# Performance work log

Measured on AMD Instinct MI355X. Metric: run time of the kernel, lower is better.

Reference implementation:

```python
import jax, jax.numpy as jnp
import numpy as np

NUM_HEADS = 6
KERNEL = 5
EPS = 1e-6


def _neighbor_idx(L, k):
    # NATTEN neighborhood: window start clamped so every query has exactly k neighbors
    starts = jnp.clip(jnp.arange(L) - k // 2, 0, L - k)
    return starts[:, None] + jnp.arange(k)  # [L, k]


def ada_rmsnorm(x, scale, w1, b1, w2, b2):
    # x: [B,C,D,H,W]; RMS over spatial dims, gamma from channel means via small MLP
    rms = jnp.sqrt(jnp.mean(x * x, axis=(2, 3, 4), keepdims=True) + EPS)
    xn = x / rms
    stats = jnp.mean(x, axis=(2, 3, 4))                 # [B,C]
    h = jax.nn.relu(stats @ w1.T + b1)                  # [B,2C]
    gamma = jax.nn.sigmoid(h @ w2.T + b2)               # [B,C]
    return xn * (scale * gamma[:, :, None, None, None])


def reference(x, scale1, n1_w1, n1_b1, n1_w2, n1_b2,
              qkv_w, qkv_b, proj_w, proj_b,
              scale2, n2_w1, n2_b1, n2_w2, n2_b2,
              mlp_w1, mlp_b1, mlp_w2, mlp_b2):
    B, C, D, H, W = x.shape
    nh_, k_ = NUM_HEADS, KERNEL
    hd = C // nh_
    K3 = k_ ** 3

    # --- norm1 + neighborhood attention ---
    h = ada_rmsnorm(x, scale1, n1_w1, n1_b1, n1_w2, n1_b2)
    t = jnp.transpose(h, (0, 2, 3, 4, 1))               # [B,D,H,W,C]
    qkv = t @ qkv_w.T + qkv_b                           # [B,D,H,W,3C]
    q, k, v = jnp.split(qkv, 3, axis=-1)
    q = q.reshape(B, D, H, W, nh_, hd)
    k = k.reshape(B, D, H, W, nh_, hd)
    v = v.reshape(B, D, H, W, nh_, hd)

    iD = _neighbor_idx(D, k_)
    iH = _neighbor_idx(H, k_)
    iW = _neighbor_idx(W, k_)
    nd = iD[:, None, None, :, None, None]               # [D,1,1,k,1,1]
    nhh = iH[None, :, None, None, :, None]              # [1,H,1,1,k,1]
    nw = iW[None, None, :, None, None, :]               # [1,1,W,1,1,k]

    k_nb = k[:, nd, nhh, nw].reshape(B, D, H, W, K3, nh_, hd)
    v_nb = v[:, nd, nhh, nw].reshape(B, D, H, W, K3, nh_, hd)

    scale_qk = hd ** -0.5
    scores = jnp.einsum('bdhwnc,bdhwknc->bdhwnk', q, k_nb) * scale_qk  # [B,D,H,W,heads,K3]
    p = jax.nn.softmax(scores, axis=-1)
    o = jnp.einsum('bdhwnk,bdhwknc->bdhwnc', p, v_nb).reshape(B, D, H, W, C)
    o = o @ proj_w.T + proj_b                            # output projection
    x = x + jnp.transpose(o, (0, 4, 1, 2, 3))

    # --- norm2 + 1x1-conv MLP (GELU exact) ---
    h2 = ada_rmsnorm(x, scale2, n2_w1, n2_b1, n2_w2, n2_b2)
    m = jnp.einsum('oc,bcdhw->bodhw', mlp_w1, h2) + mlp_b1[None, :, None, None, None]
    m = jax.nn.gelu(m, approximate=False)
    m = jnp.einsum('oc,bcdhw->bodhw', mlp_w2, m) + mlp_b2[None, :, None, None, None]
    return x + m


def setup_inputs() -> dict:
    key = jax.random.key(0)
    ks = jax.random.split(key, 16)
    B, C, D, H, W = 1, 192, 16, 16, 16
    hid = 2 * C
    mlp_h = int(4.0 * C)
    s = 0.02
    inp = {
        'x': jax.random.normal(ks[0], (B, C, D, H, W), jnp.float32),
        'scale1': jnp.ones((1, C, 1, 1, 1), jnp.float32),
        'n1_w1': jax.random.normal(ks[1], (hid, C), jnp.float32) * s,
        'n1_b1': jnp.zeros((hid,), jnp.float32),
        'n1_w2': jax.random.normal(ks[2], (C, hid), jnp.float32) * s,
        'n1_b2': jnp.zeros((C,), jnp.float32),
        'qkv_w': jax.random.normal(ks[3], (3 * C, C), jnp.float32) * s,
        'qkv_b': jnp.zeros((3 * C,), jnp.float32),
        'proj_w': jax.random.normal(ks[4], (C, C), jnp.float32) * s,
        'proj_b': jnp.zeros((C,), jnp.float32),
        'scale2': jnp.ones((1, C, 1, 1, 1), jnp.float32),
        'n2_w1': jax.random.normal(ks[5], (hid, C), jnp.float32) * s,
        'n2_b1': jnp.zeros((hid,), jnp.float32),
        'n2_w2': jax.random.normal(ks[6], (C, hid), jnp.float32) * s,
        'n2_b2': jnp.zeros((C,), jnp.float32),
        'mlp_w1': jax.random.normal(ks[7], (mlp_h, C), jnp.float32) * s,
        'mlp_b1': jnp.zeros((mlp_h,), jnp.float32),
        'mlp_w2': jax.random.normal(ks[8], (C, mlp_h), jnp.float32) * s,
        'mlp_b2': jnp.zeros((C,), jnp.float32),
    }
    return inp
```

## Files before the change

kernel.cpp:

```cpp
#include <hip/hip_runtime.h>
#include <hip/hip_bf16.h>
#include <cmath>


#define NPOS 4096
#define C_CH 192

typedef __bf16 bf16x8 __attribute__((ext_vector_type(8)));
typedef __bf16 bf16x4 __attribute__((ext_vector_type(4)));
typedef float  f32x4  __attribute__((ext_vector_type(4)));

__global__ __launch_bounds__(256) void stats_kernel(
    const float* __restrict__ x, float* __restrict__ sums, float* __restrict__ sumsq)
{
    int c = blockIdx.x;
    const float4* xc = (const float4*)(x + (size_t)c * NPOS);
    float s = 0.f, s2 = 0.f;
    for (int i = threadIdx.x; i < NPOS / 4; i += 256) {
        float4 v = xc[i];
        s  += v.x + v.y + v.z + v.w;
        s2 += v.x * v.x + v.y * v.y + v.z * v.z + v.w * v.w;
    }
    #pragma unroll
    for (int off = 32; off > 0; off >>= 1) {
        s  += __shfl_down(s, off);
        s2 += __shfl_down(s2, off);
    }
    __shared__ float ls[4], ls2[4];
    int wid = threadIdx.x >> 6;
    if ((threadIdx.x & 63) == 0) { ls[wid] = s; ls2[wid] = s2; }
    __syncthreads();
    if (threadIdx.x == 0) {
        float t = 0.f, t2 = 0.f;
        #pragma unroll
        for (int w = 0; w < 4; w++) { t += ls[w]; t2 += ls2[w]; }
        sums[c] = t; sumsq[c] = t2;
    }
}

__global__ __launch_bounds__(384) void gamma_kernel(
    const float* __restrict__ sums, const float* __restrict__ sumsq,
    const float* __restrict__ scale,
    const float* __restrict__ w1, const float* __restrict__ b1,
    const float* __restrict__ w2, const float* __restrict__ b2,
    float* __restrict__ gs)
{
    __shared__ float stats[C_CH];
    __shared__ float h[384];
    int t = threadIdx.x;
    if (t < C_CH) stats[t] = sums[t] * (1.0f / (float)NPOS);
    __syncthreads();
    {
        float acc = b1[t];
        const float* wr = w1 + (size_t)t * C_CH;
        #pragma unroll 4
        for (int c = 0; c < C_CH; c += 4) {
            float4 w4 = *(const float4*)(wr + c);
            acc += w4.x * stats[c] + w4.y * stats[c + 1] + w4.z * stats[c + 2] + w4.w * stats[c + 3];
        }
        h[t] = fmaxf(acc, 0.0f);
    }
    __syncthreads();
    if (t < C_CH) {
        float acc = b2[t];
        const float* wr = w2 + (size_t)t * 384;
        #pragma unroll 4
        for (int j = 0; j < 384; j += 4) {
            float4 w4 = *(const float4*)(wr + j);
            acc += w4.x * h[j] + w4.y * h[j + 1] + w4.z * h[j + 2] + w4.w * h[j + 3];
        }
        float g = 1.0f / (1.0f + __expf(-acc));
        float rms = sqrtf(sumsq[t] * (1.0f / (float)NPOS) + 1e-6f);
        gs[t] = scale[t] * g / rms;
    }
}

__global__ __launch_bounds__(256) void convw_kernel(
    const float* __restrict__ s0, const float* __restrict__ s1,
    const float* __restrict__ s2, const float* __restrict__ s3,
    __bf16* __restrict__ d0, __bf16* __restrict__ d1,
    __bf16* __restrict__ d2, __bf16* __restrict__ d3)
{
    int b = blockIdx.x;
    const float* s; __bf16* d; int base;
    if (b < 108)      { s = s0; d = d0; base = b; }
    else if (b < 144) { s = s1; d = d1; base = b - 108; }
    else if (b < 288) { s = s2; d = d2; base = b - 144; }
    else              { s = s3; d = d3; base = b - 288; }
    int i = (base * 256 + threadIdx.x) * 4;
    float4 v = *(const float4*)(s + i);
    bf16x4 o = { (__bf16)v.x, (__bf16)v.y, (__bf16)v.z, (__bf16)v.w };
    *(bf16x4*)(d + i) = o;
}

__global__ __launch_bounds__(256) void convx_kernel(
    const float* __restrict__ x, const float* __restrict__ gs, __bf16* __restrict__ xb)
{
    __shared__ float lds[192 * 65];
    int t = threadIdx.x;
    int p0 = blockIdx.x * 64;
    for (int idx = t; idx < 192 * 16; idx += 256) {
        int row = idx >> 4, p4 = idx & 15;
        float4 v = *(const float4*)(x + (size_t)row * NPOS + p0 + p4 * 4);
        float g = gs[row];
        lds[row * 65 + p4 * 4 + 0] = v.x * g;
        lds[row * 65 + p4 * 4 + 1] = v.y * g;
        lds[row * 65 + p4 * 4 + 2] = v.z * g;
        lds[row * 65 + p4 * 4 + 3] = v.w * g;
    }
    __syncthreads();
    for (int idx = t; idx < 48 * 64; idx += 256) {
        int c4 = idx >> 6, p = idx & 63;
        bf16x4 o;
        #pragma unroll
        for (int j = 0; j < 4; j++) o[j] = (__bf16)lds[(c4 * 4 + j) * 65 + p];
        *(bf16x4*)(xb + (size_t)(p0 + p) * 192 + c4 * 4) = o;
    }
}

template <int K, int EPI, int CFG>
__global__ __launch_bounds__(256) void mfma_gemm(
    const __bf16* __restrict__ W, const float* __restrict__ bias,
    const __bf16* __restrict__ X, void* __restrict__ out,
    const float* __restrict__ resid, int M,
    float* __restrict__ out_kv)
{
    constexpr int MT = 2;
    constexpr int NT = (CFG == 1) ? 2 : 1;
    constexpr int BM = (CFG == 1) ? 64 : 32;
    constexpr int BN = 64;
    int lane = threadIdx.x & 63;
    int wv   = threadIdx.x >> 6;
    int r16  = lane & 15;
    int quad = lane >> 4;
    int wvm = (CFG == 1) ? (wv >> 1) : 0;
    int wvn = (CFG == 1) ? (wv & 1) : wv;
    int mBase = blockIdx.y * BM + wvm * 32;
    int nBase = blockIdx.x * BN + wvn * (NT * 16);

    f32x4 acc[MT][NT];
    #pragma unroll
    for (int i = 0; i < MT; i++)
        #pragma unroll
        for (int j = 0; j < NT; j++)
            acc[i][j] = (f32x4){0.f, 0.f, 0.f, 0.f};

    const __bf16* wp = W + (size_t)(mBase + r16) * K + quad * 8;
    const __bf16* xp = X + (size_t)(nBase + r16) * K + quad * 8;

    #pragma unroll 6
    for (int ks = 0; ks < K / 32; ks++) {
        bf16x8 a[MT], b[NT];
        #pragma unroll
        for (int rt = 0; rt < MT; rt++)
            a[rt] = *(const bf16x8*)(wp + (size_t)rt * 16 * K + ks * 32);
        #pragma unroll
        for (int ct = 0; ct < NT; ct++)
            b[ct] = *(const bf16x8*)(xp + (size_t)ct * 16 * K + ks * 32);
        #pragma unroll
        for (int rt = 0; rt < MT; rt++)
            #pragma unroll
            for (int ct = 0; ct < NT; ct++)
                acc[rt][ct] = __builtin_amdgcn_mfma_f32_16x16x32_bf16(a[rt], b[ct], acc[rt][ct], 0, 0, 0);
    }

    #pragma unroll
    for (int rt = 0; rt < MT; rt++) {
        int m0 = mBase + rt * 16 + quad * 4;
        float b0 = bias[m0], b1 = bias[m0 + 1], b2 = bias[m0 + 2], b3 = bias[m0 + 3];
        #pragma unroll
        for (int ct = 0; ct < NT; ct++) {
            int n = nBase + ct * 16 + r16;
            f32x4 a4 = acc[rt][ct];
            float g0 = a4[0] + b0, g1 = a4[1] + b1, g2 = a4[2] + b2, g3 = a4[3] + b3;
            if (EPI == 0) {
                int sect = m0 / 192;
                int o0 = m0 - sect * 192;
                if (sect == 0) {
                    const float qs = 0.17677669529663687f;
                    *(float4*)((float*)out + (size_t)n * 192 + o0) =
                        make_float4(g0 * qs, g1 * qs, g2 * qs, g3 * qs);
                } else {
                    float* dst = out_kv + (size_t)n * 384 + (sect - 1) * 192 + o0;
                    *(float4*)dst = make_float4(g0, g1, g2, g3);
                }
            } else if (EPI == 2) {
                float* o = (float*)out;
                size_t i0 = (size_t)m0 * NPOS + n;
                o[i0]            = g0 + resid[i0];
                o[i0 + NPOS]     = g1 + resid[i0 + NPOS];
                o[i0 + 2 * NPOS] = g2 + resid[i0 + 2 * NPOS];
                o[i0 + 3 * NPOS] = g3 + resid[i0 + 3 * NPOS];
            } else {
                bf16x4 v;
                v[0] = (__bf16)(0.5f * g0 * (1.0f + erff(g0 * 0.7071067811865475f)));
                v[1] = (__bf16)(0.5f * g1 * (1.0f + erff(g1 * 0.7071067811865475f)));
                v[2] = (__bf16)(0.5f * g2 * (1.0f + erff(g2 * 0.7071067811865475f)));
                v[3] = (__bf16)(0.5f * g3 * (1.0f + erff(g3 * 0.7071067811865475f)));
                *(bf16x4*)((__bf16*)out + (size_t)n * M + m0) = v;
            }
        }
    }
}

__global__ __launch_bounds__(256) void attn_kernel(
    const float* __restrict__ q, const float* __restrict__ kv, __bf16* __restrict__ o)
{
    int t = threadIdx.x;
    int pairIdx = blockIdx.x * 8 + (t >> 5);
    int sg   = (t >> 3) & 3;
    int lane = t & 7;
    int pos = pairIdx / 6;
    int head = pairIdx - pos * 6;
    int wq = pos & 15;
    int hq = (pos >> 4) & 15;
    int dq = pos >> 8;
    int d0 = min(max(dq - 2, 0), 11);
    int h0 = min(max(hq - 2, 0), 11);
    int w0 = min(max(wq - 2, 0), 11);

    const float* kvb = kv + head * 32 + lane * 4;
    float4 q4 = *(const float4*)(q + (size_t)pos * 192 + head * 32 + lane * 4);

    float l = 0.0f;
    float4 acc = make_float4(0.f, 0.f, 0.f, 0.f);

    for (int dh = sg; dh < 25; dh += 4) {
        int di = dh / 5;
        int hi = dh - di * 5;
        int np0 = (d0 + di) * 256 + (h0 + hi) * 16 + w0;
        const float* p = kvb + (size_t)np0 * 384;
        #pragma unroll
        for (int wi = 0; wi < 5; wi++) {
            float4 k4 = *(const float4*)p;
            float4 v4 = *(const float4*)(p + 192);
            float s = q4.x * k4.x + q4.y * k4.y + q4.z * k4.z + q4.w * k4.w;
            s += __shfl_xor(s, 1);
            s += __shfl_xor(s, 2);
            s += __shfl_xor(s, 4);
            float pr = __expf(s);
            l += pr;
            acc.x += pr * v4.x;
            acc.y += pr * v4.y;
            acc.z += pr * v4.z;
            acc.w += pr * v4.w;
            p += 384;
        }
    }

    #pragma unroll
    for (int off = 8; off <= 16; off <<= 1) {
        l     += __shfl_xor(l, off);
        acc.x += __shfl_xor(acc.x, off);
        acc.y += __shfl_xor(acc.y, off);
        acc.z += __shfl_xor(acc.z, off);
        acc.w += __shfl_xor(acc.w, off);
    }

    if (sg == 0) {
        float rl = 1.0f / l;
        bf16x4 ov = { (__bf16)(acc.x * rl), (__bf16)(acc.y * rl),
                      (__bf16)(acc.z * rl), (__bf16)(acc.w * rl) };
        *(bf16x4*)(o + (size_t)pos * 192 + head * 32 + lane * 4) = ov;
    }
}

extern "C" void kernel_launch(void* const* d_in, const int* in_sizes, int n_in,
                              void* d_out, int out_size, void* d_ws, size_t ws_size,
                              hipStream_t stream)
{
    const float* x      = (const float*)d_in[0];
    const float* scale1 = (const float*)d_in[1];
    const float* n1_w1  = (const float*)d_in[2];
    const float* n1_b1  = (const float*)d_in[3];
    const float* n1_w2  = (const float*)d_in[4];
    const float* n1_b2  = (const float*)d_in[5];
    const float* qkv_w  = (const float*)d_in[6];
    const float* qkv_b  = (const float*)d_in[7];
    const float* proj_w = (const float*)d_in[8];
    const float* proj_b = (const float*)d_in[9];
    const float* scale2 = (const float*)d_in[10];
    const float* n2_w1  = (const float*)d_in[11];
    const float* n2_b1  = (const float*)d_in[12];
    const float* n2_w2  = (const float*)d_in[13];
    const float* n2_b2  = (const float*)d_in[14];
    const float* mlp_w1 = (const float*)d_in[15];
    const float* mlp_b1 = (const float*)d_in[16];
    const float* mlp_w2 = (const float*)d_in[17];
    const float* mlp_b2 = (const float*)d_in[18];

    float* ws = (float*)d_ws;
    float*  q_buf  = ws;
    float*  kv_buf = ws + 786432;
    __bf16* m_buf  = (__bf16*)ws;
    __bf16* xb     = (__bf16*)(ws + 2359296);
    __bf16* o_attn = (__bf16*)(ws + 2752512);
    __bf16* qkv_wb = (__bf16*)(ws + 3145728);
    __bf16* proj_wb = qkv_wb + 110592;
    __bf16* m1_wb   = proj_wb + 36864;
    __bf16* m2_wb   = m1_wb + 147456;
    float*  sums   = ws + 3366912;
    float*  sumsq  = sums + 192;
    float*  gsv    = sums + 384;

    float* x2 = (float*)d_out;

    convw_kernel<<<432, 256, 0, stream>>>(qkv_w, proj_w, mlp_w1, mlp_w2,
                                          qkv_wb, proj_wb, m1_wb, m2_wb);
    stats_kernel<<<192, 256, 0, stream>>>(x, sums, sumsq);
    gamma_kernel<<<1, 384, 0, stream>>>(sums, sumsq, scale1, n1_w1, n1_b1, n1_w2, n1_b2, gsv);
    convx_kernel<<<64, 256, 0, stream>>>(x, gsv, xb);
    mfma_gemm<192, 0, 1><<<dim3(64, 9), 256, 0, stream>>>(qkv_wb, qkv_b, xb, (void*)q_buf, nullptr, 576, kv_buf);
    attn_kernel<<<3072, 256, 0, stream>>>(q_buf, kv_buf, o_attn);
    mfma_gemm<192, 2, 2><<<dim3(64, 6), 256, 0, stream>>>(proj_wb, proj_b, o_attn, (void*)x2, x, 192, nullptr);
    stats_kernel<<<192, 256, 0, stream>>>(x2, sums, sumsq);
    gamma_kernel<<<1, 384, 0, stream>>>(sums, sumsq, scale2, n2_w1, n2_b1, n2_w2, n2_b2, gsv);
    convx_kernel<<<64, 256, 0, stream>>>(x2, gsv, xb);
    mfma_gemm<192, 3, 1><<<dim3(64, 12), 256, 0, stream>>>(m1_wb, mlp_b1, xb, (void*)m_buf, nullptr, 768, nullptr);
    mfma_gemm<768, 2, 2><<<dim3(64, 6), 256, 0, stream>>>(m2_wb, mlp_b2, m_buf, (void*)x2, x2, 192, nullptr);
}
```

Measured before the change: 232.1 us.

## Fuse prep kernels, recompute gamma per block, store K/V in bf16

Result: no change. 230.1 us (-0.9%).

```diff
diff --git a/kernel.cpp b/kernel.cpp
--- a/kernel.cpp
+++ b/kernel.cpp
@@ -10,25 +10,70 @@
 typedef __bf16 bf16x4 __attribute__((ext_vector_type(4)));
 typedef float  f32x4  __attribute__((ext_vector_type(4)));
 
+__global__ __launch_bounds__(256) void prep_kernel(
+    const float* __restrict__ s0, const float* __restrict__ s1,
+    const float* __restrict__ s2, const float* __restrict__ s3,
+    __bf16* __restrict__ d0, __bf16* __restrict__ d1,
+    __bf16* __restrict__ d2, __bf16* __restrict__ d3,
+    const float* __restrict__ x, float* __restrict__ sums, float* __restrict__ sumsq)
+{
+    int b = blockIdx.x;
+    if (b < 432) {
+        const float* src; __bf16* dst; int base;
+        if (b < 108)      { src = s0; dst = d0; base = b; }
+        else if (b < 144) { src = s1; dst = d1; base = b - 108; }
+        else if (b < 288) { src = s2; dst = d2; base = b - 144; }
+        else              { src = s3; dst = d3; base = b - 288; }
+        int i = (base * 256 + threadIdx.x) * 4;
+        float4 v = *(const float4*)(src + i);
+        bf16x4 o = { (__bf16)v.x, (__bf16)v.y, (__bf16)v.z, (__bf16)v.w };
+        *(bf16x4*)(dst + i) = o;
+        return;
+    }
+    int c = b - 432;
+    const float4* xc = (const float4*)(x + (size_t)c * NPOS);
+    float a = 0.f, a2 = 0.f;
+    for (int i = threadIdx.x; i < NPOS / 4; i += 256) {
+        float4 v = xc[i];
+        a  += v.x + v.y + v.z + v.w;
+        a2 += v.x * v.x + v.y * v.y + v.z * v.z + v.w * v.w;
+    }
+    #pragma unroll
+    for (int off = 32; off > 0; off >>= 1) {
+        a  += __shfl_down(a, off);
+        a2 += __shfl_down(a2, off);
+    }
+    __shared__ float ls[4], ls2[4];
+    int wid = threadIdx.x >> 6;
+    if ((threadIdx.x & 63) == 0) { ls[wid] = a; ls2[wid] = a2; }
+    __syncthreads();
+    if (threadIdx.x == 0) {
+        float t = 0.f, t2 = 0.f;
+        #pragma unroll
+        for (int w = 0; w < 4; w++) { t += ls[w]; t2 += ls2[w]; }
+        sums[c] = t; sumsq[c] = t2;
+    }
+}
+
 __global__ __launch_bounds__(256) void stats_kernel(
     const float* __restrict__ x, float* __restrict__ sums, float* __restrict__ sumsq)
 {
     int c = blockIdx.x;
     const float4* xc = (const float4*)(x + (size_t)c * NPOS);
-    float s = 0.f, s2 = 0.f;
+    float a = 0.f, a2 = 0.f;
     for (int i = threadIdx.x; i < NPOS / 4; i += 256) {
         float4 v = xc[i];
-        s  += v.x + v.y + v.z + v.w;
-        s2 += v.x * v.x + v.y * v.y + v.z * v.z + v.w * v.w;
+        a  += v.x + v.y + v.z + v.w;
+        a2 += v.x * v.x + v.y * v.y + v.z * v.z + v.w * v.w;
     }
     #pragma unroll
     for (int off = 32; off > 0; off >>= 1) {
-        s  += __shfl_down(s, off);
-        s2 += __shfl_down(s2, off);
+        a  += __shfl_down(a, off);
+        a2 += __shfl_down(a2, off);
     }
     __shared__ float ls[4], ls2[4];
     int wid = threadIdx.x >> 6;
-    if ((threadIdx.x & 63) == 0) { ls[wid] = s; ls2[wid] = s2; }
+    if ((threadIdx.x & 63) == 0) { ls[wid] = a; ls2[wid] = a2; }
     __syncthreads();
     if (threadIdx.x == 0) {
         float t = 0.f, t2 = 0.f;
@@ -38,27 +83,31 @@
     }
 }
 
-__global__ __launch_bounds__(384) void gamma_kernel(
+__global__ __launch_bounds__(256) void convx_kernel(
+    const float* __restrict__ x,
     const float* __restrict__ sums, const float* __restrict__ sumsq,
     const float* __restrict__ scale,
     const float* __restrict__ w1, const float* __restrict__ b1,
     const float* __restrict__ w2, const float* __restrict__ b2,
-    float* __restrict__ gs)
+    __bf16* __restrict__ xb)
 {
     __shared__ float stats[C_CH];
     __shared__ float h[384];
+    __shared__ float gsl[C_CH];
+    __shared__ float lds[192 * 65];
     int t = threadIdx.x;
+
     if (t < C_CH) stats[t] = sums[t] * (1.0f / (float)NPOS);
     __syncthreads();
-    {
-        float acc = b1[t];
-        const float* wr = w1 + (size_t)t * C_CH;
+    for (int j = t; j < 384; j += 256) {
+        float acc = b1[j];
+        const float* wr = w1 + (size_t)j * C_CH;
         #pragma unroll 4
         for (int c = 0; c < C_CH; c += 4) {
             float4 w4 = *(const float4*)(wr + c);
             acc += w4.x * stats[c] + w4.y * stats[c + 1] + w4.z * stats[c + 2] + w4.w * stats[c + 3];
         }
-        h[t] = fmaxf(acc, 0.0f);
+        h[j] = fmaxf(acc, 0.0f);
     }
     __syncthreads();
     if (t < C_CH) {
@@ -71,38 +120,15 @@
         }
         float g = 1.0f / (1.0f + __expf(-acc));
         float rms = sqrtf(sumsq[t] * (1.0f / (float)NPOS) + 1e-6f);
-        gs[t] = scale[t] * g / rms;
-    }
-}
-
-__global__ __launch_bounds__(256) void convw_kernel(
-    const float* __restrict__ s0, const float* __restrict__ s1,
-    const float* __restrict__ s2, const float* __restrict__ s3,
-    __bf16* __restrict__ d0, __bf16* __restrict__ d1,
-    __bf16* __restrict__ d2, __bf16* __restrict__ d3)
-{
-    int b = blockIdx.x;
-    const float* s; __bf16* d; int base;
-    if (b < 108)      { s = s0; d = d0; base = b; }
-    else if (b < 144) { s = s1; d = d1; base = b - 108; }
-    else if (b < 288) { s = s2; d = d2; base = b - 144; }
-    else              { s = s3; d = d3; base = b - 288; }
-    int i = (base * 256 + threadIdx.x) * 4;
-    float4 v = *(const float4*)(s + i);
-    bf16x4 o = { (__bf16)v.x, (__bf16)v.y, (__bf16)v.z, (__bf16)v.w };
-    *(bf16x4*)(d + i) = o;
-}
-
-__global__ __launch_bounds__(256) void convx_kernel(
-    const float* __restrict__ x, const float* __restrict__ gs, __bf16* __restrict__ xb)
-{
-    __shared__ float lds[192 * 65];
-    int t = threadIdx.x;
+        gsl[t] = scale[t] * g / rms;
+    }
+    __syncthreads();
+
     int p0 = blockIdx.x * 64;
     for (int idx = t; idx < 192 * 16; idx += 256) {
         int row = idx >> 4, p4 = idx & 15;
         float4 v = *(const float4*)(x + (size_t)row * NPOS + p0 + p4 * 4);
-        float g = gs[row];
+        float g = gsl[row];
         lds[row * 65 + p4 * 4 + 0] = v.x * g;
         lds[row * 65 + p4 * 4 + 1] = v.y * g;
         lds[row * 65 + p4 * 4 + 2] = v.z * g;
@@ -123,7 +149,7 @@
     const __bf16* __restrict__ W, const float* __restrict__ bias,
     const __bf16* __restrict__ X, void* __restrict__ out,
     const float* __restrict__ resid, int M,
-    float* __restrict__ out_kv)
+    __bf16* __restrict__ out_kv)
 {
     constexpr int MT = 2;
     constexpr int NT = (CFG == 1) ? 2 : 1;
@@ -181,8 +207,8 @@
                     *(float4*)((float*)out + (size_t)n * 192 + o0) =
                         make_float4(g0 * qs, g1 * qs, g2 * qs, g3 * qs);
                 } else {
-                    float* dst = out_kv + (size_t)n * 384 + (sect - 1) * 192 + o0;
-                    *(float4*)dst = make_float4(g0, g1, g2, g3);
+                    bf16x4 v = { (__bf16)g0, (__bf16)g1, (__bf16)g2, (__bf16)g3 };
+                    *(bf16x4*)(out_kv + (size_t)n * 384 + (sect - 1) * 192 + o0) = v;
                 }
             } else if (EPI == 2) {
                 float* o = (float*)out;
@@ -204,7 +230,7 @@
 }
 
 __global__ __launch_bounds__(256) void attn_kernel(
-    const float* __restrict__ q, const float* __restrict__ kv, __bf16* __restrict__ o)
+    const float* __restrict__ q, const __bf16* __restrict__ kv, __bf16* __restrict__ o)
 {
     int t = threadIdx.x;
     int pairIdx = blockIdx.x * 8 + (t >> 5);
@@ -219,7 +245,7 @@
     int h0 = min(max(hq - 2, 0), 11);
     int w0 = min(max(wq - 2, 0), 11);
 
-    const float* kvb = kv + head * 32 + lane * 4;
+    const __bf16* kvb = kv + head * 32 + lane * 4;
     float4 q4 = *(const float4*)(q + (size_t)pos * 192 + head * 32 + lane * 4);
 
     float l = 0.0f;
@@ -229,21 +255,25 @@
         int di = dh / 5;
         int hi = dh - di * 5;
         int np0 = (d0 + di) * 256 + (h0 + hi) * 16 + w0;
-        const float* p = kvb + (size_t)np0 * 384;
+        const __bf16* p = kvb + (size_t)np0 * 384;
         #pragma unroll
         for (int wi = 0; wi < 5; wi++) {
-            float4 k4 = *(const float4*)p;
-            float4 v4 = *(const float4*)(p + 192);
-            float s = q4.x * k4.x + q4.y * k4.y + q4.z * k4.z + q4.w * k4.w;
+            uint2 kk = *(const uint2*)p;
+            uint2 vv = *(const uint2*)(p + 192);
+            float k0 = __uint_as_float(kk.x << 16);
+            float k1 = __uint_as_float(kk.x & 0xFFFF0000u);
+            float k2 = __uint_as_float(kk.y << 16);
+            float k3 = __uint_as_float(kk.y & 0xFFFF0000u);
+            float s = q4.x * k0 + q4.y * k1 + q4.z * k2 + q4.w * k3;
             s += __shfl_xor(s, 1);
             s += __shfl_xor(s, 2);
             s += __shfl_xor(s, 4);
             float pr = __expf(s);
             l += pr;
-            acc.x += pr * v4.x;
-            acc.y += pr * v4.y;
-            acc.z += pr * v4.z;
-            acc.w += pr * v4.w;
+            acc.x += pr * __uint_as_float(vv.x << 16);
+            acc.y += pr * __uint_as_float(vv.x & 0xFFFF0000u);
+            acc.z += pr * __uint_as_float(vv.y << 16);
+            acc.w += pr * __uint_as_float(vv.y & 0xFFFF0000u);
             p += 384;
         }
     }
@@ -291,7 +321,7 @@
 
     float* ws = (float*)d_ws;
     float*  q_buf  = ws;
-    float*  kv_buf = ws + 786432;
+    __bf16* kv_buf = (__bf16*)(ws + 786432);
     __bf16* m_buf  = (__bf16*)ws;
     __bf16* xb     = (__bf16*)(ws + 2359296);
     __bf16* o_attn = (__bf16*)(ws + 2752512);
@@ -301,21 +331,20 @@
     __bf16* m2_wb   = m1_wb + 147456;
     float*  sums   = ws + 3366912;
     float*  sumsq  = sums + 192;
-    float*  gsv    = sums + 384;
 
     float* x2 = (float*)d_out;
 
-    convw_kernel<<<432, 256, 0, stream>>>(qkv_w, proj_w, mlp_w1, mlp_w2,
-                                          qkv_wb, proj_wb, m1_wb, m2_wb);
-    stats_kernel<<<192, 256, 0, stream>>>(x, sums, sumsq);
-    gamma_kernel<<<1, 384, 0, stream>>>(sums, sumsq, scale1, n1_w1, n1_b1, n1_w2, n1_b2, gsv);
-    convx_kernel<<<64, 256, 0, stream>>>(x, gsv, xb);
+    prep_kernel<<<624, 256, 0, stream>>>(qkv_w, proj_w, mlp_w1, mlp_w2,
+                                         qkv_wb, proj_wb, m1_wb, m2_wb,
+                                         x, sums, sumsq);
+    convx_kernel<<<64, 256, 0, stream>>>(x, sums, sumsq, scale1,
+                                         n1_w1, n1_b1, n1_w2, n1_b2, xb);
     mfma_gemm<192, 0, 1><<<dim3(64, 9), 256, 0, stream>>>(qkv_wb, qkv_b, xb, (void*)q_buf, nullptr, 576, kv_buf);
     attn_kernel<<<3072, 256, 0, stream>>>(q_buf, kv_buf, o_attn);
     mfma_gemm<192, 2, 2><<<dim3(64, 6), 256, 0, stream>>>(proj_wb, proj_b, o_attn, (void*)x2, x, 192, nullptr);
     stats_kernel<<<192, 256, 0, stream>>>(x2, sums, sumsq);
-    gamma_kernel<<<1, 384, 0, stream>>>(sums, sumsq, scale2, n2_w1, n2_b1, n2_w2, n2_b2, gsv);
-    convx_kernel<<<64, 256, 0, stream>>>(x2, gsv, xb);
+    convx_kernel<<<64, 256, 0, stream>>>(x2, sums, sumsq, scale2,
+                                         n2_w1, n2_b1, n2_w2, n2_b2, xb);
     mfma_gemm<192, 3, 1><<<dim3(64, 12), 256, 0, stream>>>(m1_wb, mlp_b1, xb, (void*)m_buf, nullptr, 768, nullptr);
     mfma_gemm<768, 2, 2><<<dim3(64, 6), 256, 0, stream>>>(m2_wb, mlp_b2, m_buf, (void*)x2, x2, 192, nullptr);
 }
```
